# Kernel optimization log

Measured on AMD Instinct MI355X. Metric: run time of the kernel, lower is better.

## Reference

```python
import jax, jax.numpy as jnp
import numpy as np

N = 12288
E = N * 32  # avg degree 32


def spmm(row, col, w, support):
    # out[i] = sum_{e: row[e]==i} w[e] * support[col[e]]
    return jax.ops.segment_sum(w[:, None] * support[col], row, num_segments=N)


def setup_inputs() -> dict:
    key = jax.random.key(0)
    ks = jax.random.split(key, 7)
    x = jax.random.normal(ks[0], (N, 512), dtype=jnp.float32)
    edge_row = jax.random.randint(ks[1], (E,), 0, N, dtype=jnp.int32)
    edge_col = jax.random.randint(ks[2], (E,), 0, N, dtype=jnp.int32)
    # row-normalized-ish positive edge weights
    edge_w = jax.random.uniform(ks[3], (E,), dtype=jnp.float32) / 32.0
    def xavier(k, fan_in, fan_out):
        bound = float(np.sqrt(6.0 / (fan_in + fan_out)))
        return jax.random.uniform(k, (fan_in, fan_out), jnp.float32, -bound, bound)
    W1 = xavier(ks[4], 512, 256)
    W2 = xavier(ks[5], 256, 128)
    W3 = xavier(ks[6], 128, 64)
    return {"x": x, "edge_row": edge_row, "edge_col": edge_col,
            "edge_w": edge_w, "W1": W1, "W2": W2, "W3": W3}


def reference(x, edge_row, edge_col, edge_w, W1, W2, W3):
    # GNNLayer 1 (active=True): tanh(x @ W) then spmm(adj, .)
    z1 = spmm(edge_row, edge_col, edge_w, jnp.tanh(x @ W1))
    # GNNLayer 2 (active=True)
    z2 = spmm(edge_row, edge_col, edge_w, jnp.tanh(z1 @ W2))
    # GNNLayer 3 (active=False): no activation
    z_igae = spmm(edge_row, edge_col, edge_w, z2 @ W3)  # [N, 64]
    # reconstructed adjacency: sigmoid(z z^T), [N, N]
    z_igae_adj = jax.nn.sigmoid(z_igae @ z_igae.T)
    return (z_igae, z_igae_adj)
```

## Files before the change

kernel.cpp:

```cpp
#include <hip/hip_runtime.h>
#include <hip/hip_bf16.h>

#define NNODES 12288
#define NEDGES (NNODES * 32)
#define ELLCAP 128

typedef __attribute__((ext_vector_type(4))) float f32x4;
typedef __attribute__((ext_vector_type(8))) __bf16 bf16x8;

__global__ __launch_bounds__(256) void prep_kernel(const float* __restrict__ W1,
                                                   const float* __restrict__ W2,
                                                   const float* __restrict__ W3,
                                                   __bf16* __restrict__ W1t,
                                                   __bf16* __restrict__ W2t,
                                                   __bf16* __restrict__ W3t,
                                                   int* __restrict__ deg) {
    int i = blockIdx.x * 256 + threadIdx.x;
    if (i < NNODES) { deg[i] = 0; return; }
    int j = i - NNODES;
    if (j < 512 * 256) { W1t[(size_t)(j % 256) * 512 + j / 256] = (__bf16)W1[j]; return; }
    j -= 512 * 256;
    if (j < 256 * 128) { W2t[(size_t)(j % 128) * 256 + j / 128] = (__bf16)W2[j]; return; }
    j -= 256 * 128;
    if (j < 128 * 64) { W3t[(size_t)(j % 64) * 128 + j / 64] = (__bf16)W3[j]; return; }
}

__global__ __launch_bounds__(256) void scatter_ell(const int* __restrict__ row,
                                                   const int* __restrict__ col,
                                                   const float* __restrict__ w,
                                                   int* __restrict__ deg,
                                                   int2* __restrict__ ell) {
    int e = blockIdx.x * 256 + threadIdx.x;
    int r = row[e];
    int p = atomicAdd(&deg[r], 1);
    int2 cw; cw.x = col[e]; cw.y = __float_as_int(w[e]);
    ell[(size_t)r * ELLCAP + p] = cw;
}

template <bool TANH, int K, bool A_F32>
__global__ __launch_bounds__(256) void gemm_mfma(const void* __restrict__ Av,
                                                 const __bf16* __restrict__ Wt,
                                                 __bf16* __restrict__ C, int Nc) {
    int wave = threadIdx.x >> 6, lane = threadIdx.x & 63;
    int lr = lane & 15;
    int kg = lane >> 4;
    int m0 = blockIdx.x * 128 + wave * 32;
    int n0 = blockIdx.y * 64;
    f32x4 acc[2][4];
#pragma unroll
    for (int mi = 0; mi < 2; mi++)
#pragma unroll
        for (int ni = 0; ni < 4; ni++) acc[mi][ni] = (f32x4){0.f, 0.f, 0.f, 0.f};
#pragma unroll
    for (int k0 = 0; k0 < K; k0 += 32) {
        bf16x8 af[2], bf[4];
#pragma unroll
        for (int mi = 0; mi < 2; mi++) {
            if (A_F32) {
                const float* ap = (const float*)Av + (size_t)(m0 + mi * 16 + lr) * K + k0 + kg * 8;
                f32x4 a0 = *(const f32x4*)ap;
                f32x4 a1 = *(const f32x4*)(ap + 4);
#pragma unroll
                for (int j = 0; j < 4; j++) { af[mi][j] = (__bf16)a0[j]; af[mi][4 + j] = (__bf16)a1[j]; }
            } else {
                af[mi] = *(const bf16x8*)((const __bf16*)Av + (size_t)(m0 + mi * 16 + lr) * K + k0 + kg * 8);
            }
        }
#pragma unroll
        for (int ni = 0; ni < 4; ni++)
            bf[ni] = *(const bf16x8*)(Wt + (size_t)(n0 + ni * 16 + lr) * K + k0 + kg * 8);
#pragma unroll
        for (int mi = 0; mi < 2; mi++)
#pragma unroll
            for (int ni = 0; ni < 4; ni++)
                acc[mi][ni] = __builtin_amdgcn_mfma_f32_16x16x32_bf16(af[mi], bf[ni], acc[mi][ni], 0, 0, 0);
    }
#pragma unroll
    for (int mi = 0; mi < 2; mi++)
#pragma unroll
        for (int ni = 0; ni < 4; ni++) {
            int col = n0 + ni * 16 + lr;
            int rowb = m0 + mi * 16 + kg * 4;
#pragma unroll
            for (int r = 0; r < 4; r++) {
                float v = acc[mi][ni][r];
                if (TANH) v = tanhf(v);
                C[(size_t)(rowb + r) * Nc + col] = (__bf16)v;
            }
        }
}

template <int K, int NOUT, bool TANH>
__global__ __launch_bounds__(16 * K / 8) void fused_spmm_gemm(const int* __restrict__ deg,
                                                              const int2* __restrict__ ell,
                                                              const __bf16* __restrict__ h_in,
                                                              const __bf16* __restrict__ Wt,
                                                              __bf16* __restrict__ h_out) {
    constexpr int L = K / 8;
    __shared__ __bf16 zs[16][K + 4];
    int tid = threadIdx.x;
    int rloc = tid / L;
    int f8 = (tid % L) * 8;
    int rglob = blockIdx.x * 16 + rloc;
    int d = deg[rglob];
    const int2* er = ell + (size_t)rglob * ELLCAP;
    float acc[8] = {};
#pragma unroll 8
    for (int e = 0; e < d; e++) {
        int2 cw = er[e];
        float w = __int_as_float(cw.y);
        bf16x8 hv = *(const bf16x8*)(h_in + (size_t)cw.x * K + f8);
#pragma unroll
        for (int j = 0; j < 8; j++) acc[j] = fmaf(w, (float)hv[j], acc[j]);
    }
    bf16x8 o;
#pragma unroll
    for (int j = 0; j < 8; j++) o[j] = (__bf16)acc[j];
    *(bf16x8*)&zs[rloc][f8] = o;
    __syncthreads();
    int wave = tid >> 6, lane = tid & 63;
    int lr = lane & 15, kg = lane >> 4;
    f32x4 c = (f32x4){0.f, 0.f, 0.f, 0.f};
#pragma unroll
    for (int ks = 0; ks < K / 32; ks++) {
        bf16x8 a = *(const bf16x8*)&zs[lr][ks * 32 + kg * 8];
        bf16x8 b = *(const bf16x8*)(Wt + (size_t)(wave * 16 + lr) * K + ks * 32 + kg * 8);
        c = __builtin_amdgcn_mfma_f32_16x16x32_bf16(a, b, c, 0, 0, 0);
    }
#pragma unroll
    for (int r = 0; r < 4; r++) {
        float v = c[r];
        if (TANH) v = tanhf(v);
        h_out[(size_t)(blockIdx.x * 16 + kg * 4 + r) * NOUT + wave * 16 + lr] = (__bf16)v;
    }
}

__global__ __launch_bounds__(256) void spmm_final(const int* __restrict__ deg,
                                                  const int2* __restrict__ ell,
                                                  const __bf16* __restrict__ h,
                                                  __bf16* __restrict__ z,
                                                  float* __restrict__ zf) {
    int r = blockIdx.x * 32 + threadIdx.x / 8;
    int f8 = (threadIdx.x & 7) * 8;
    int d = deg[r];
    const int2* er = ell + (size_t)r * ELLCAP;
    float acc[8] = {};
#pragma unroll 8
    for (int e = 0; e < d; e++) {
        int2 cw = er[e];
        float w = __int_as_float(cw.y);
        bf16x8 hv = *(const bf16x8*)(h + (size_t)cw.x * 64 + f8);
#pragma unroll
        for (int j = 0; j < 8; j++) acc[j] = fmaf(w, (float)hv[j], acc[j]);
    }
    bf16x8 o;
#pragma unroll
    for (int j = 0; j < 8; j++) o[j] = (__bf16)acc[j];
    *(bf16x8*)(z + (size_t)r * 64 + f8) = o;
    f32x4 o0, o1;
#pragma unroll
    for (int j = 0; j < 4; j++) { o0[j] = acc[j]; o1[j] = acc[4 + j]; }
    *(f32x4*)(zf + (size_t)r * 64 + f8) = o0;
    *(f32x4*)(zf + (size_t)r * 64 + f8 + 4) = o1;
}

__global__ __launch_bounds__(256) void zzt_sigmoid(const __bf16* __restrict__ Z,
                                                   float* __restrict__ out) {
    __shared__ float tile[32][260];
    int wave = threadIdx.x >> 6;
    int lane = threadIdx.x & 63;
    int lr = lane & 15;
    int kg = lane >> 4;
    int r0 = blockIdx.y * 64;
    int c0blk = blockIdx.x * 256;
    int c0 = c0blk + wave * 64;
    bf16x8 af[4][2], bfr[4][2];
#pragma unroll
    for (int i = 0; i < 4; i++)
#pragma unroll
        for (int ks = 0; ks < 2; ks++) {
            af[i][ks]  = *(const bf16x8*)(Z + (size_t)(r0 + i * 16 + lr) * 64 + ks * 32 + kg * 8);
            bfr[i][ks] = *(const bf16x8*)(Z + (size_t)(c0 + i * 16 + lr) * 64 + ks * 32 + kg * 8);
        }
    f32x4 acc[4][4];
#pragma unroll
    for (int mi = 0; mi < 4; mi++)
#pragma unroll
        for (int ni = 0; ni < 4; ni++) acc[mi][ni] = (f32x4){0.f, 0.f, 0.f, 0.f};
#pragma unroll
    for (int mi = 0; mi < 4; mi++)
#pragma unroll
        for (int ni = 0; ni < 4; ni++) {
            acc[mi][ni] = __builtin_amdgcn_mfma_f32_16x16x32_bf16(af[mi][0], bfr[ni][0], acc[mi][ni], 0, 0, 0);
            acc[mi][ni] = __builtin_amdgcn_mfma_f32_16x16x32_bf16(af[mi][1], bfr[ni][1], acc[mi][ni], 0, 0, 0);
        }
#pragma unroll
    for (int ph = 0; ph < 2; ph++) {
#pragma unroll
        for (int mi2 = 0; mi2 < 2; mi2++) {
            int mi = ph * 2 + mi2;
#pragma unroll
            for (int ni = 0; ni < 4; ni++) {
                int colb = wave * 64 + ni * 16 + lr;
                int rowl = mi2 * 16 + kg * 4;
#pragma unroll
                for (int r = 0; r < 4; r++) {
                    float e = __expf(-acc[mi][ni][r]);
                    tile[rowl + r][colb] = __builtin_amdgcn_rcpf(1.f + e);
                }
            }
        }
        __syncthreads();
#pragma unroll
        for (int it = 0; it < 8; it++) {
            int rowl = it * 4 + wave;
            size_t grow = (size_t)(r0 + ph * 32 + rowl);
            *(f32x4*)(out + grow * NNODES + c0blk + lane * 4) = *(const f32x4*)&tile[rowl][lane * 4];
        }
        __syncthreads();
    }
}

extern "C" void kernel_launch(void* const* d_in, const int* in_sizes, int n_in,
                              void* d_out, int out_size, void* d_ws, size_t ws_size,
                              hipStream_t stream) {
    (void)in_sizes; (void)n_in; (void)out_size; (void)ws_size;
    const float* x  = (const float*)d_in[0];
    const int* erow = (const int*)d_in[1];
    const int* ecol = (const int*)d_in[2];
    const float* ew = (const float*)d_in[3];
    const float* W1 = (const float*)d_in[4];
    const float* W2 = (const float*)d_in[5];
    const float* W3 = (const float*)d_in[6];
    float* z_igae = (float*)d_out;
    float* adj = (float*)d_out + (size_t)NNODES * 64;

    char* ws = (char*)d_ws;
    size_t off = 0;
    auto alloc = [&](size_t bytes) {
        void* p = ws + off;
        off += (bytes + 255) & ~(size_t)255;
        return p;
    };
    __bf16* W1t = (__bf16*)alloc((size_t)512 * 256 * 2);
    __bf16* W2t = (__bf16*)alloc((size_t)256 * 128 * 2);
    __bf16* W3t = (__bf16*)alloc((size_t)128 * 64 * 2);
    __bf16* h1  = (__bf16*)alloc((size_t)NNODES * 256 * 2);
    __bf16* h2  = (__bf16*)alloc((size_t)NNODES * 128 * 2);
    __bf16* h3  = (__bf16*)alloc((size_t)NNODES * 64 * 2);
    __bf16* Zb  = (__bf16*)alloc((size_t)NNODES * 64 * 2);
    int* deg    = (int*)alloc(NNODES * 4);
    int2* ell   = (int2*)alloc((size_t)NNODES * ELLCAP * 8);

    prep_kernel<<<(NNODES + 512 * 256 + 256 * 128 + 128 * 64 + 255) / 256, 256, 0, stream>>>(
        W1, W2, W3, W1t, W2t, W3t, deg);
    scatter_ell<<<NEDGES / 256, 256, 0, stream>>>(erow, ecol, ew, deg, ell);

    gemm_mfma<true, 512, true><<<dim3(NNODES / 128, 256 / 64), 256, 0, stream>>>(x, W1t, h1, 256);
    fused_spmm_gemm<256, 128, true><<<NNODES / 16, 512, 0, stream>>>(deg, ell, h1, W2t, h2);
    fused_spmm_gemm<128, 64, false><<<NNODES / 16, 256, 0, stream>>>(deg, ell, h2, W3t, h3);
    spmm_final<<<NNODES / 32, 256, 0, stream>>>(deg, ell, h3, Zb, z_igae);
    zzt_sigmoid<<<dim3(NNODES / 256, NNODES / 64), 256, 0, stream>>>((const __bf16*)Zb, adj);
}
```

Before: 234.5 us.

## Merge edge scatter into first GEMM launch and double-buffer sigmoid tile stores

The ELL scatter and the first dense GEMM now run as one launch: the first 384 blocks do the GEMM and the rest do the edge scatter. This removes a kernel launch and lets the two independent stages overlap on the GPU. The zzt_sigmoid epilogue now writes 16-row chunks through a ping-pong shared tile, so the sigmoid for the next chunk can overlap with the global stores of the current one. The cost is more barriers and a smaller tile per phase in the output kernel, which dominates runtime because of the large N×N write.

```diff
diff --git a/kernel.cpp b/kernel.cpp
--- a/kernel.cpp
+++ b/kernel.cpp
@@ -25,27 +25,27 @@
     if (j < 128 * 64) { W3t[(size_t)(j % 64) * 128 + j / 64] = (__bf16)W3[j]; return; }
 }
 
-__global__ __launch_bounds__(256) void scatter_ell(const int* __restrict__ row,
-                                                   const int* __restrict__ col,
-                                                   const float* __restrict__ w,
-                                                   int* __restrict__ deg,
-                                                   int2* __restrict__ ell) {
-    int e = blockIdx.x * 256 + threadIdx.x;
-    int r = row[e];
-    int p = atomicAdd(&deg[r], 1);
-    int2 cw; cw.x = col[e]; cw.y = __float_as_int(w[e]);
-    ell[(size_t)r * ELLCAP + p] = cw;
-}
-
-template <bool TANH, int K, bool A_F32>
-__global__ __launch_bounds__(256) void gemm_mfma(const void* __restrict__ Av,
-                                                 const __bf16* __restrict__ Wt,
-                                                 __bf16* __restrict__ C, int Nc) {
+__global__ __launch_bounds__(256) void gemm1_scatter(const float* __restrict__ x,
+                                                     const __bf16* __restrict__ W1t,
+                                                     __bf16* __restrict__ h1,
+                                                     const int* __restrict__ erow,
+                                                     const int* __restrict__ ecol,
+                                                     const float* __restrict__ ew,
+                                                     int* __restrict__ deg,
+                                                     int2* __restrict__ ell) {
+    if (blockIdx.x >= 384) {
+        int e = (blockIdx.x - 384) * 256 + threadIdx.x;
+        int r = erow[e];
+        int p = atomicAdd(&deg[r], 1);
+        int2 cw; cw.x = ecol[e]; cw.y = __float_as_int(ew[e]);
+        ell[(size_t)r * ELLCAP + p] = cw;
+        return;
+    }
+    constexpr int K = 512, Nc = 256;
     int wave = threadIdx.x >> 6, lane = threadIdx.x & 63;
-    int lr = lane & 15;
-    int kg = lane >> 4;
-    int m0 = blockIdx.x * 128 + wave * 32;
-    int n0 = blockIdx.y * 64;
+    int lr = lane & 15, kg = lane >> 4;
+    int m0 = (blockIdx.x % 96) * 128 + wave * 32;
+    int n0 = (blockIdx.x / 96) * 64;
     f32x4 acc[2][4];
 #pragma unroll
     for (int mi = 0; mi < 2; mi++)
@@ -56,19 +56,15 @@
         bf16x8 af[2], bf[4];
 #pragma unroll
         for (int mi = 0; mi < 2; mi++) {
-            if (A_F32) {
-                const float* ap = (const float*)Av + (size_t)(m0 + mi * 16 + lr) * K + k0 + kg * 8;
-                f32x4 a0 = *(const f32x4*)ap;
-                f32x4 a1 = *(const f32x4*)(ap + 4);
-#pragma unroll
-                for (int j = 0; j < 4; j++) { af[mi][j] = (__bf16)a0[j]; af[mi][4 + j] = (__bf16)a1[j]; }
-            } else {
-                af[mi] = *(const bf16x8*)((const __bf16*)Av + (size_t)(m0 + mi * 16 + lr) * K + k0 + kg * 8);
-            }
+            const float* ap = x + (size_t)(m0 + mi * 16 + lr) * K + k0 + kg * 8;
+            f32x4 a0 = *(const f32x4*)ap;
+            f32x4 a1 = *(const f32x4*)(ap + 4);
+#pragma unroll
+            for (int j = 0; j < 4; j++) { af[mi][j] = (__bf16)a0[j]; af[mi][4 + j] = (__bf16)a1[j]; }
         }
 #pragma unroll
         for (int ni = 0; ni < 4; ni++)
-            bf[ni] = *(const bf16x8*)(Wt + (size_t)(n0 + ni * 16 + lr) * K + k0 + kg * 8);
+            bf[ni] = *(const bf16x8*)(W1t + (size_t)(n0 + ni * 16 + lr) * K + k0 + kg * 8);
 #pragma unroll
         for (int mi = 0; mi < 2; mi++)
 #pragma unroll
@@ -82,11 +78,8 @@
             int col = n0 + ni * 16 + lr;
             int rowb = m0 + mi * 16 + kg * 4;
 #pragma unroll
-            for (int r = 0; r < 4; r++) {
-                float v = acc[mi][ni][r];
-                if (TANH) v = tanhf(v);
-                C[(size_t)(rowb + r) * Nc + col] = (__bf16)v;
-            }
+            for (int r = 0; r < 4; r++)
+                h1[(size_t)(rowb + r) * Nc + col] = (__bf16)tanhf(acc[mi][ni][r]);
         }
 }
 
@@ -166,7 +159,7 @@
 
 __global__ __launch_bounds__(256) void zzt_sigmoid(const __bf16* __restrict__ Z,
                                                    float* __restrict__ out) {
-    __shared__ float tile[32][260];
+    __shared__ float tile[2][16][260];
     int wave = threadIdx.x >> 6;
     int lane = threadIdx.x & 63;
     int lr = lane & 15;
@@ -195,27 +188,33 @@
             acc[mi][ni] = __builtin_amdgcn_mfma_f32_16x16x32_bf16(af[mi][1], bfr[ni][1], acc[mi][ni], 0, 0, 0);
         }
 #pragma unroll
-    for (int ph = 0; ph < 2; ph++) {
-#pragma unroll
-        for (int mi2 = 0; mi2 < 2; mi2++) {
-            int mi = ph * 2 + mi2;
+    for (int ni = 0; ni < 4; ni++) {
+        int colb = wave * 64 + ni * 16 + lr;
+#pragma unroll
+        for (int r = 0; r < 4; r++) {
+            float e = __expf(-acc[0][ni][r]);
+            tile[0][kg * 4 + r][colb] = __builtin_amdgcn_rcpf(1.f + e);
+        }
+    }
+    __syncthreads();
+#pragma unroll
+    for (int p = 0; p < 4; p++) {
+        if (p < 3) {
 #pragma unroll
             for (int ni = 0; ni < 4; ni++) {
                 int colb = wave * 64 + ni * 16 + lr;
-                int rowl = mi2 * 16 + kg * 4;
 #pragma unroll
                 for (int r = 0; r < 4; r++) {
-                    float e = __expf(-acc[mi][ni][r]);
-                    tile[rowl + r][colb] = __builtin_amdgcn_rcpf(1.f + e);
+                    float e = __expf(-acc[p + 1][ni][r]);
+                    tile[(p + 1) & 1][kg * 4 + r][colb] = __builtin_amdgcn_rcpf(1.f + e);
                 }
             }
         }
-        __syncthreads();
-#pragma unroll
-        for (int it = 0; it < 8; it++) {
+#pragma unroll
+        for (int it = 0; it < 4; it++) {
             int rowl = it * 4 + wave;
-            size_t grow = (size_t)(r0 + ph * 32 + rowl);
-            *(f32x4*)(out + grow * NNODES + c0blk + lane * 4) = *(const f32x4*)&tile[rowl][lane * 4];
+            size_t grow = (size_t)(r0 + p * 16 + rowl);
+            *(f32x4*)(out + grow * NNODES + c0blk + lane * 4) = *(const f32x4*)&tile[p & 1][rowl][lane * 4];
         }
         __syncthreads();
     }
@@ -254,9 +253,7 @@
 
     prep_kernel<<<(NNODES + 512 * 256 + 256 * 128 + 128 * 64 + 255) / 256, 256, 0, stream>>>(
         W1, W2, W3, W1t, W2t, W3t, deg);
-    scatter_ell<<<NEDGES / 256, 256, 0, stream>>>(erow, ecol, ew, deg, ell);
-
-    gemm_mfma<true, 512, true><<<dim3(NNODES / 128, 256 / 64), 256, 0, stream>>>(x, W1t, h1, 256);
+    gemm1_scatter<<<384 + NEDGES / 256, 256, 0, stream>>>(x, W1t, h1, erow, ecol, ew, deg, ell);
     fused_spmm_gemm<256, 128, true><<<NNODES / 16, 512, 0, stream>>>(deg, ell, h1, W2t, h2);
     fused_spmm_gemm<128, 64, false><<<NNODES / 16, 256, 0, stream>>>(deg, ell, h2, W3t, h3);
     spmm_final<<<NNODES / 32, 256, 0, stream>>>(deg, ell, h3, Zb, z_igae);
```

Result: no change. 230.1 us (-1.9%).
